# Kernel tuning notes

Measured on AMD Instinct MI355X. Metric: run time of the kernel, lower is better.

Reference implementation:

```python
import jax, jax.numpy as jnp
import numpy as np

DIM = 128  # matches init kwarg `dim`; scale = dim ** 0.5


def setup_inputs() -> dict:
    key = jax.random.key(0)
    k1, k2, k3, k4 = jax.random.split(key, 4)
    A = 100000
    K = 1600000  # num edges
    z_msg_all = jax.random.normal(k1, (A, DIM), dtype=jnp.float32)
    recv_query_all = jax.random.normal(k2, (A, DIM), dtype=jnp.float32)
    i_idx = jax.random.randint(k3, (K,), 0, A, dtype=jnp.int64)
    j_idx = jax.random.randint(k4, (K,), 0, A, dtype=jnp.int64)
    return {"z_msg_all": z_msg_all, "recv_query_all": recv_query_all,
            "i_idx": i_idx, "j_idx": j_idx, "A": A}


def reference(z_msg_all, recv_query_all, i_idx, j_idx, A):
    # q_j = z[j], k_i = z[i]; per-edge scores; segmented softmax over recipient j;
    # weighted scatter-add of values k_i into pooled[j]. recv_query_all is unused
    # in the original forward (kept for signature fidelity).
    scale = DIM ** 0.5
    k = z_msg_all[i_idx]                     # (K, D) gather
    q = z_msg_all[j_idx]                     # (K, D) gather
    scores = jnp.sum(q * k, axis=-1) / scale  # (K,)
    # segmented softmax (3-pass: amax, exp, sum)
    max_per = jax.ops.segment_max(scores, j_idx, num_segments=A)  # (A,)
    exp = jnp.exp(scores - max_per[j_idx])                         # (K,)
    denom = jax.ops.segment_sum(exp, j_idx, num_segments=A)        # (A,)
    alpha = exp / (denom[j_idx] + 1e-6)                            # (K,)
    # weighted scatter-add of values into recipients
    pooled = jax.ops.segment_sum(alpha[:, None] * k, j_idx, num_segments=A)  # (A, D)
    return pooled
```

## Files before the change

kernel.cpp:

```cpp
#include <hip/hip_runtime.h>
#include <math.h>


typedef _Float16 h2 __attribute__((ext_vector_type(2)));

#define CAP   8192
#define ABLK  512
#define EPB   (ABLK * 8)

__device__ inline h2 as_h2(unsigned u) { return __builtin_bit_cast(h2, u); }

__global__ __launch_bounds__(ABLK) void bin_kernel(
        const float* __restrict__ z, uint4* __restrict__ z16,
        const int* __restrict__ i_idx, const int* __restrict__ j_idx,
        int* __restrict__ gcount, unsigned* __restrict__ binned,
        int n16, int K, int NB) {
    int tid = threadIdx.x;
    int t0 = blockIdx.x * ABLK + tid;
    int nth = gridDim.x * ABLK;

    {
        const float4* __restrict__ z4 = reinterpret_cast<const float4*>(z);
        #pragma unroll
        for (int q = 0; q < 8; ++q) {
            int t = t0 + q * nth;
            if (t < n16) {
                float4 a = z4[(size_t)2 * t];
                float4 c = z4[(size_t)2 * t + 1];
                uint4 o;
                o.x = __builtin_bit_cast(unsigned, __builtin_amdgcn_cvt_pkrtz(a.x, a.y));
                o.y = __builtin_bit_cast(unsigned, __builtin_amdgcn_cvt_pkrtz(a.z, a.w));
                o.z = __builtin_bit_cast(unsigned, __builtin_amdgcn_cvt_pkrtz(c.x, c.y));
                o.w = __builtin_bit_cast(unsigned, __builtin_amdgcn_cvt_pkrtz(c.z, c.w));
                z16[t] = o;
            }
        }
    }

    __shared__ int lhist[ABLK];
    __shared__ int loff[ABLK + 1];
    __shared__ int lcur[ABLK];
    __shared__ int gbase[ABLK];
    __shared__ unsigned staged_p[EPB];
    __shared__ unsigned short staged_b[EPB];

    lhist[tid] = 0;
    __syncthreads();

    int ebase = blockIdx.x * EPB;
    int myi[8], myj[8], myb[8];
    #pragma unroll
    for (int q = 0; q < 8; ++q) {
        int e = ebase + tid + q * ABLK;
        if (e < K) {
            myj[q] = j_idx[e];
            myi[q] = i_idx[e];
            myb[q] = myj[q] >> 8;
            atomicAdd(&lhist[myb[q]], 1);
        } else {
            myb[q] = -1;
        }
    }
    __syncthreads();
    for (int off = 1; off < ABLK; off <<= 1) {
        int v = (tid >= off) ? lhist[tid - off] : 0;
        __syncthreads();
        lhist[tid] += v;
        __syncthreads();
    }
    loff[tid + 1] = lhist[tid];
    if (tid == 0) loff[0] = 0;
    __syncthreads();
    int cntb = loff[tid + 1] - loff[tid];
    if (tid < NB && cntb > 0)
        gbase[tid] = tid * CAP + atomicAdd(&gcount[tid], cntb);
    lcur[tid] = loff[tid];
    __syncthreads();
    #pragma unroll
    for (int q = 0; q < 8; ++q) {
        if (myb[q] >= 0) {
            int p = atomicAdd(&lcur[myb[q]], 1);
            staged_p[p] = ((unsigned)myi[q] << 8) | ((unsigned)myj[q] & 255u);
            staged_b[p] = (unsigned short)myb[q];
        }
    }
    __syncthreads();
    int totE = loff[ABLK];
    for (int idx = tid; idx < totE; idx += ABLK) {
        int bb = staged_b[idx];
        binned[(size_t)gbase[bb] + (idx - loff[bb])] = staged_p[idx];
    }
}

__global__ __launch_bounds__(1024) void finish_kernel(
        unsigned* __restrict__ binned, const int* __restrict__ gcount,
        int2* __restrict__ seg, int A) {
    __shared__ unsigned staged[CAP];
    __shared__ int sorted_loc[CAP];
    __shared__ int hist[256];
    __shared__ int offs[257];
    __shared__ int cur[256];

    int b = blockIdx.x;
    int tid = threadIdx.x;
    int cnt = gcount[b];
    if (cnt > CAP) cnt = CAP;
    unsigned* __restrict__ src = binned + (size_t)b * CAP;

    if (tid < 256) hist[tid] = 0;
    for (int x = tid; x < cnt; x += 1024) staged[x] = src[x];
    __syncthreads();
    for (int x = tid; x < cnt; x += 1024)
        atomicAdd(&hist[staged[x] & 255u], 1);
    __syncthreads();
    for (int off = 1; off < 256; off <<= 1) {
        int v = 0;
        if (tid < 256 && tid >= off) v = hist[tid - off];
        __syncthreads();
        if (tid < 256 && tid >= off) hist[tid] += v;
        __syncthreads();
    }
    if (tid == 0) offs[0] = 0;
    if (tid < 256) offs[tid + 1] = hist[tid];
    __syncthreads();
    if (tid < 256) cur[tid] = offs[tid];
    __syncthreads();
    for (int x = tid; x < cnt; x += 1024) {
        unsigned pk = staged[x];
        int p = atomicAdd(&cur[pk & 255u], 1);
        sorted_loc[p] = (int)(pk >> 8);
    }
    __syncthreads();
    for (int x = tid; x < cnt; x += 1024) src[x] = (unsigned)sorted_loc[x];
    if (tid < 256) {
        int j = (b << 8) + tid;
        if (j < A)
            seg[j] = make_int2(b * CAP + offs[tid], b * CAP + offs[tid + 1]);
    }
}

__global__ __launch_bounds__(256, 8) void attn_kernel(
        const uint4* __restrict__ zk,
        const unsigned* __restrict__ sorted_i, const int2* __restrict__ seg,
        float* __restrict__ out, int A) {
    int w = blockIdx.x * 4 + (threadIdx.x >> 6);
    if (w >= A) return;
    int lane = threadIdx.x & 63;
    int g = lane >> 3;
    int r = lane & 7;

    const float kscale = 0.08838834764831843f * 1.4426950408889634f;

    uint4 uq0 = zk[(size_t)w * 16 + r];
    uint4 uq1 = zk[(size_t)w * 16 + 8 + r];
    h2 qh[8];
    qh[0] = as_h2(uq0.x); qh[1] = as_h2(uq0.y);
    qh[2] = as_h2(uq0.z); qh[3] = as_h2(uq0.w);
    qh[4] = as_h2(uq1.x); qh[5] = as_h2(uq1.y);
    qh[6] = as_h2(uq1.z); qh[7] = as_h2(uq1.w);

    int2 s01 = seg[w];

    float l = 0.0f;
    float acc[16];
    #pragma unroll
    for (int d = 0; d < 16; ++d) acc[d] = 0.0f;

    int p = s01.x + g;
    unsigned i0 = sorted_i[p];
    i0 = (i0 < (unsigned)A) ? i0 : 0u;
    uint4 u0 = zk[(size_t)i0 * 16 + r];
    uint4 u1 = zk[(size_t)i0 * 16 + 8 + r];
    unsigned i1 = sorted_i[p + 8];
    i1 = (i1 < (unsigned)A) ? i1 : 0u;

    while (p < s01.y) {
        uint4 n0 = zk[(size_t)i1 * 16 + r];
        uint4 n1 = zk[(size_t)i1 * 16 + 8 + r];
        unsigned i2 = sorted_i[p + 16];
        i2 = (i2 < (unsigned)A) ? i2 : 0u;

        h2 kh[8];
        kh[0] = as_h2(u0.x); kh[1] = as_h2(u0.y);
        kh[2] = as_h2(u0.z); kh[3] = as_h2(u0.w);
        kh[4] = as_h2(u1.x); kh[5] = as_h2(u1.y);
        kh[6] = as_h2(u1.z); kh[7] = as_h2(u1.w);

        float pa = __builtin_amdgcn_fdot2(qh[0], kh[0], 0.0f, false);
        float pb = __builtin_amdgcn_fdot2(qh[4], kh[4], 0.0f, false);
        pa = __builtin_amdgcn_fdot2(qh[1], kh[1], pa, false);
        pb = __builtin_amdgcn_fdot2(qh[5], kh[5], pb, false);
        pa = __builtin_amdgcn_fdot2(qh[2], kh[2], pa, false);
        pb = __builtin_amdgcn_fdot2(qh[6], kh[6], pb, false);
        pa = __builtin_amdgcn_fdot2(qh[3], kh[3], pa, false);
        pb = __builtin_amdgcn_fdot2(qh[7], kh[7], pb, false);
        float part = pa + pb;
        part += __shfl_xor(part, 1);
        part += __shfl_xor(part, 2);
        part += __shfl_xor(part, 4);

        float pe = exp2f(part * kscale);
        l += pe;
        #pragma unroll
        for (int t = 0; t < 8; ++t) {
            acc[2 * t]     = fmaf(pe, (float)kh[t].x, acc[2 * t]);
            acc[2 * t + 1] = fmaf(pe, (float)kh[t].y, acc[2 * t + 1]);
        }
        u0 = n0; u1 = n1; i1 = i2;
        p += 8;
    }

    l += __shfl_xor(l, 8);
    l += __shfl_xor(l, 16);
    l += __shfl_xor(l, 32);

    {
        bool hi = (g & 4) != 0;
        #pragma unroll
        for (int t = 0; t < 4; ++t) {
            float sx = hi ? acc[2 * t]     : acc[2 * t + 8];
            float sy = hi ? acc[2 * t + 1] : acc[2 * t + 9];
            float rx = __shfl_xor(sx, 32);
            float ry = __shfl_xor(sy, 32);
            float kx = hi ? acc[2 * t + 8] : acc[2 * t];
            float ky = hi ? acc[2 * t + 9] : acc[2 * t + 1];
            acc[2 * t]     = kx + rx;
            acc[2 * t + 1] = ky + ry;
        }
        hi = (g & 2) != 0;
        #pragma unroll
        for (int t = 0; t < 2; ++t) {
            float sx = hi ? acc[2 * t]     : acc[2 * t + 4];
            float sy = hi ? acc[2 * t + 1] : acc[2 * t + 5];
            float rx = __shfl_xor(sx, 16);
            float ry = __shfl_xor(sy, 16);
            float kx = hi ? acc[2 * t + 4] : acc[2 * t];
            float ky = hi ? acc[2 * t + 5] : acc[2 * t + 1];
            acc[2 * t]     = kx + rx;
            acc[2 * t + 1] = ky + ry;
        }
        hi = (g & 1) != 0;
        {
            float sx = hi ? acc[0] : acc[2];
            float sy = hi ? acc[1] : acc[3];
            float rx = __shfl_xor(sx, 8);
            float ry = __shfl_xor(sy, 8);
            float kx = hi ? acc[2] : acc[0];
            float ky = hi ? acc[3] : acc[1];
            acc[0] = kx + rx;
            acc[1] = ky + ry;
        }
    }

    float inv = 1.0f / (l + 1e-6f);
    float2 o;
    o.x = acc[0] * inv;
    o.y = acc[1] * inv;
    int o_idx = ((g & 4) << 3) + 4 * r + (g & 3);
    reinterpret_cast<float2*>(out)[(size_t)w * 64 + o_idx] = o;
}

extern "C" void kernel_launch(void* const* d_in, const int* in_sizes, int n_in,
                              void* d_out, int out_size, void* d_ws, size_t ws_size,
                              hipStream_t stream) {
    const float* z     = (const float*)d_in[0];
    const int*   i_idx = (const int*)d_in[2];
    const int*   j_idx = (const int*)d_in[3];

    const int D = 128;
    int A = in_sizes[0] / D;
    int K = in_sizes[2];
    int n16 = A * (D / 8);
    int NB = (A + 255) >> 8;

    unsigned short* z16 = (unsigned short*)d_ws;
    unsigned* binned = (unsigned*)(z16 + (size_t)A * 128);
    int2* seg = (int2*)(binned + (size_t)NB * CAP);
    int* gcount = (int*)(seg + A);

    float* out = (float*)d_out;

    (void)hipMemsetAsync(gcount, 0, (size_t)NB * sizeof(int), stream);
    int gA = (K + EPB - 1) / EPB;
    int gC = (n16 + EPB - 1) / EPB;
    if (gC > gA) gA = gC;
    bin_kernel<<<gA, ABLK, 0, stream>>>(z, (uint4*)z16, i_idx, j_idx,
                                        gcount, binned, n16, K, NB);
    finish_kernel<<<NB, 1024, 0, stream>>>(binned, gcount, seg, A);
    attn_kernel<<<(A + 3) / 4, 256, 0, stream>>>((const uint4*)z16, binned,
                                                 seg, out, A);
}
```

Measured before the change: 104.3 us.

## Deepen attention gather prefetch and use wave-shuffle scans in binning kernels

The attention loop now prefetches key rows two iterations ahead instead of one, and drops the per-index bounds clamp. To keep the speculative reads safe, finish_kernel zero-pads the 32 slots after each bin's entries. The bin and finish kernels replace their barrier-heavy Hillis-Steele shared-memory scans with wavefront shuffle scans plus a small cross-wave pass, and bin_kernel loads edge indices as int4 vectors. The deeper prefetch uses more registers, which could lower occupancy, and out-of-range prefetch indices now rely on the zero padding being present.

```diff
diff --git a/kernel.cpp b/kernel.cpp
--- a/kernel.cpp
+++ b/kernel.cpp
@@ -16,11 +16,13 @@
         int* __restrict__ gcount, unsigned* __restrict__ binned,
         int n16, int K, int NB) {
     int tid = threadIdx.x;
-    int t0 = blockIdx.x * ABLK + tid;
-    int nth = gridDim.x * ABLK;
+    int lane = tid & 63;
+    int wid = tid >> 6;
 
     {
         const float4* __restrict__ z4 = reinterpret_cast<const float4*>(z);
+        int nth = gridDim.x * ABLK;
+        int t0 = blockIdx.x * ABLK + tid;
         #pragma unroll
         for (int q = 0; q < 8; ++q) {
             int t = t0 + q * nth;
@@ -38,9 +40,12 @@
     }
 
     __shared__ int lhist[ABLK];
-    __shared__ int loff[ABLK + 1];
+    __shared__ int loff[ABLK];
     __shared__ int lcur[ABLK];
     __shared__ int gbase[ABLK];
+    __shared__ int wtot[8];
+    __shared__ int wexc[8];
+    __shared__ int totE_sh;
     __shared__ unsigned staged_p[EPB];
     __shared__ unsigned short staged_b[EPB];
 
@@ -50,11 +55,25 @@
     int ebase = blockIdx.x * EPB;
     int myi[8], myj[8], myb[8];
     #pragma unroll
+    for (int h = 0; h < 2; ++h) {
+        int e0 = ebase + 4 * (tid + h * ABLK);
+        if (e0 + 3 < K) {
+            int4 jv = *reinterpret_cast<const int4*>(j_idx + e0);
+            int4 iv = *reinterpret_cast<const int4*>(i_idx + e0);
+            myj[4*h+0] = jv.x; myj[4*h+1] = jv.y; myj[4*h+2] = jv.z; myj[4*h+3] = jv.w;
+            myi[4*h+0] = iv.x; myi[4*h+1] = iv.y; myi[4*h+2] = iv.z; myi[4*h+3] = iv.w;
+        } else {
+            #pragma unroll
+            for (int c = 0; c < 4; ++c) {
+                int e = e0 + c;
+                if (e < K) { myj[4*h+c] = j_idx[e]; myi[4*h+c] = i_idx[e]; }
+                else       { myj[4*h+c] = -1; }
+            }
+        }
+    }
+    #pragma unroll
     for (int q = 0; q < 8; ++q) {
-        int e = ebase + tid + q * ABLK;
-        if (e < K) {
-            myj[q] = j_idx[e];
-            myi[q] = i_idx[e];
+        if (myj[q] >= 0) {
             myb[q] = myj[q] >> 8;
             atomicAdd(&lhist[myb[q]], 1);
         } else {
@@ -62,20 +81,30 @@
         }
     }
     __syncthreads();
-    for (int off = 1; off < ABLK; off <<= 1) {
-        int v = (tid >= off) ? lhist[tid - off] : 0;
-        __syncthreads();
-        lhist[tid] += v;
-        __syncthreads();
-    }
-    loff[tid + 1] = lhist[tid];
-    if (tid == 0) loff[0] = 0;
-    __syncthreads();
-    int cntb = loff[tid + 1] - loff[tid];
-    if (tid < NB && cntb > 0)
-        gbase[tid] = tid * CAP + atomicAdd(&gcount[tid], cntb);
-    lcur[tid] = loff[tid];
-    __syncthreads();
+
+    int v = lhist[tid];
+    int incl = v;
+    #pragma unroll
+    for (int off = 1; off < 64; off <<= 1) {
+        int t = __shfl_up(incl, off);
+        if (lane >= off) incl += t;
+    }
+    if (lane == 63) wtot[wid] = incl;
+    __syncthreads();
+    if (tid < 8) {
+        int s = 0;
+        for (int k2 = 0; k2 < tid; ++k2) s += wtot[k2];
+        wexc[tid] = s;
+    }
+    __syncthreads();
+    int excl = wexc[wid] + incl - v;
+    loff[tid] = excl;
+    lcur[tid] = excl;
+    if (tid == ABLK - 1) totE_sh = excl + v;
+    if (tid < NB && v > 0)
+        gbase[tid] = tid * CAP + atomicAdd(&gcount[tid], v);
+    __syncthreads();
+
     #pragma unroll
     for (int q = 0; q < 8; ++q) {
         if (myb[q] >= 0) {
@@ -85,7 +114,7 @@
         }
     }
     __syncthreads();
-    int totE = loff[ABLK];
+    int totE = totE_sh;
     for (int idx = tid; idx < totE; idx += ABLK) {
         int bb = staged_b[idx];
         binned[(size_t)gbase[bb] + (idx - loff[bb])] = staged_p[idx];
@@ -100,9 +129,12 @@
     __shared__ int hist[256];
     __shared__ int offs[257];
     __shared__ int cur[256];
+    __shared__ int wtot4[4];
+    __shared__ int wexc4[4];
 
     int b = blockIdx.x;
     int tid = threadIdx.x;
+    int lane = tid & 63;
     int cnt = gcount[b];
     if (cnt > CAP) cnt = CAP;
     unsigned* __restrict__ src = binned + (size_t)b * CAP;
@@ -113,17 +145,31 @@
     for (int x = tid; x < cnt; x += 1024)
         atomicAdd(&hist[staged[x] & 255u], 1);
     __syncthreads();
-    for (int off = 1; off < 256; off <<= 1) {
-        int v = 0;
-        if (tid < 256 && tid >= off) v = hist[tid - off];
-        __syncthreads();
-        if (tid < 256 && tid >= off) hist[tid] += v;
-        __syncthreads();
-    }
-    if (tid == 0) offs[0] = 0;
-    if (tid < 256) offs[tid + 1] = hist[tid];
-    __syncthreads();
-    if (tid < 256) cur[tid] = offs[tid];
+
+    int v = 0, incl = 0;
+    if (tid < 256) {
+        v = hist[tid];
+        incl = v;
+        #pragma unroll
+        for (int off = 1; off < 64; off <<= 1) {
+            int t = __shfl_up(incl, off);
+            if (lane >= off) incl += t;
+        }
+        if (lane == 63) wtot4[tid >> 6] = incl;
+    }
+    __syncthreads();
+    if (tid < 4) {
+        int s = 0;
+        for (int k2 = 0; k2 < tid; ++k2) s += wtot4[k2];
+        wexc4[tid] = s;
+    }
+    __syncthreads();
+    if (tid < 256) {
+        int excl = wexc4[tid >> 6] + incl - v;
+        offs[tid] = excl;
+        cur[tid] = excl;
+        if (tid == 255) offs[256] = excl + v;
+    }
     __syncthreads();
     for (int x = tid; x < cnt; x += 1024) {
         unsigned pk = staged[x];
@@ -132,6 +178,7 @@
     }
     __syncthreads();
     for (int x = tid; x < cnt; x += 1024) src[x] = (unsigned)sorted_loc[x];
+    if (tid < 32 && cnt + 32 <= CAP) src[cnt + tid] = 0u;
     if (tid < 256) {
         int j = (b << 8) + tid;
         if (j < A)
@@ -160,6 +207,7 @@
     qh[6] = as_h2(uq1.z); qh[7] = as_h2(uq1.w);
 
     int2 s01 = seg[w];
+    int end = s01.y;
 
     float l = 0.0f;
     float acc[16];
@@ -167,24 +215,24 @@
     for (int d = 0; d < 16; ++d) acc[d] = 0.0f;
 
     int p = s01.x + g;
-    unsigned i0 = sorted_i[p];
-    i0 = (i0 < (unsigned)A) ? i0 : 0u;
-    uint4 u0 = zk[(size_t)i0 * 16 + r];
-    uint4 u1 = zk[(size_t)i0 * 16 + 8 + r];
-    unsigned i1 = sorted_i[p + 8];
-    i1 = (i1 < (unsigned)A) ? i1 : 0u;
-
-    while (p < s01.y) {
-        uint4 n0 = zk[(size_t)i1 * 16 + r];
-        uint4 n1 = zk[(size_t)i1 * 16 + 8 + r];
-        unsigned i2 = sorted_i[p + 16];
-        i2 = (i2 < (unsigned)A) ? i2 : 0u;
+    unsigned iA = sorted_i[p];
+    unsigned iB = sorted_i[p + 8];
+    uint4 A0 = zk[(size_t)iA * 16 + r];
+    uint4 A1 = zk[(size_t)iA * 16 + 8 + r];
+    uint4 B0 = zk[(size_t)iB * 16 + r];
+    uint4 B1 = zk[(size_t)iB * 16 + 8 + r];
+    unsigned iC = sorted_i[p + 16];
+
+    while (p < end) {
+        uint4 C0 = zk[(size_t)iC * 16 + r];
+        uint4 C1 = zk[(size_t)iC * 16 + 8 + r];
+        unsigned iD = sorted_i[p + 24];
 
         h2 kh[8];
-        kh[0] = as_h2(u0.x); kh[1] = as_h2(u0.y);
-        kh[2] = as_h2(u0.z); kh[3] = as_h2(u0.w);
-        kh[4] = as_h2(u1.x); kh[5] = as_h2(u1.y);
-        kh[6] = as_h2(u1.z); kh[7] = as_h2(u1.w);
+        kh[0] = as_h2(A0.x); kh[1] = as_h2(A0.y);
+        kh[2] = as_h2(A0.z); kh[3] = as_h2(A0.w);
+        kh[4] = as_h2(A1.x); kh[5] = as_h2(A1.y);
+        kh[6] = as_h2(A1.z); kh[7] = as_h2(A1.w);
 
         float pa = __builtin_amdgcn_fdot2(qh[0], kh[0], 0.0f, false);
         float pb = __builtin_amdgcn_fdot2(qh[4], kh[4], 0.0f, false);
@@ -206,7 +254,8 @@
             acc[2 * t]     = fmaf(pe, (float)kh[t].x, acc[2 * t]);
             acc[2 * t + 1] = fmaf(pe, (float)kh[t].y, acc[2 * t + 1]);
         }
-        u0 = n0; u1 = n1; i1 = i2;
+
+        A0 = B0; A1 = B1; B0 = C0; B1 = C1; iC = iD;
         p += 8;
     }
 
```

Result: faster. 101.9 us (-2.2%).
